# Performance work log

Hardware: AMD Instinct MI355X
Metric: run time of the kernel (lower is better)

Reference implementation:

```python
import jax, jax.numpy as jnp
import numpy as np

N = 50000
E = 800000
D_IN = 64
D_H = 64


def setup_inputs() -> dict:
    key = jax.random.key(0)
    k1, k2, k3, k4 = jax.random.split(key, 4)
    x = jax.random.normal(k1, (N, D_IN), dtype=jnp.float32)
    edge_index = jax.random.randint(k2, (2, E), 0, N, dtype=jnp.int32)
    W1 = jax.random.normal(k3, (D_IN, D_H), dtype=jnp.float32) * (1.0 / np.sqrt(D_IN))
    b1 = jnp.zeros((D_H,), dtype=jnp.float32)
    W2 = jax.random.normal(k4, (D_H, 1), dtype=jnp.float32) * (1.0 / np.sqrt(D_H))
    b2 = jnpp = jnp.zeros((1,), dtype=jnp.float32)
    return {"x": x, "edge_index": edge_index, "W1": W1, "b1": b1, "W2": W2, "b2": b2}


def reference(x, edge_index, W1, b1, W2, b2):
    n = x.shape[0]
    # dgl.add_self_loop: append (i, i) edges for every node
    loops = jnp.arange(n, dtype=edge_index.dtype)
    src = jnp.concatenate([edge_index[0], loops])
    dst = jnp.concatenate([edge_index[1], loops])

    ones = jnp.ones(src.shape[0], dtype=x.dtype)
    deg_out = jax.ops.segment_sum(ones, src, num_segments=n)  # out-degree (src side)
    deg_in = jax.ops.segment_sum(ones, dst, num_segments=n)   # in-degree (dst side)
    # norm='both': symmetric D^{-1/2} A D^{-1/2}; zero where degree is zero (DGL sets inf->0)
    norm_src = jnp.where(deg_out > 0, jax.lax.rsqrt(deg_out), 0.0)[:, None]
    norm_dst = jnp.where(deg_in > 0, jax.lax.rsqrt(deg_in), 0.0)[:, None]

    def aggregate(h):
        # degree-normalized sparse neighbor sum (SpMM via gather + segment_sum)
        h = h * norm_src
        m = jax.ops.segment_sum(h[src], dst, num_segments=n)
        return m * norm_dst

    # layer 1 (in_feats == h_feats -> aggregate first, then transform), bias after agg
    h = aggregate(x) @ W1 + b1
    h = jax.nn.relu(h)
    # layer 2 (in_feats > out_feats -> transform first, then aggregate), bias at end
    out = aggregate(h @ W2) + b2
    return out  # [N, 1]
```

## Files before the change

kernel.cpp:

```cpp
#include <hip/hip_runtime.h>


constexpr int D = 64;
constexpr int NODE_TILE = 12800;
constexpr int NCHUNK = 64;
constexpr int HTH = 1024;

typedef float f32x8 __attribute__((ext_vector_type(8)));

__device__ __forceinline__ int rl_i(int v, int l) { return __builtin_amdgcn_readlane(v, l); }
__device__ __forceinline__ float rl_f(float v, int l) {
    return __builtin_bit_cast(float, __builtin_amdgcn_readlane(__builtin_bit_cast(int, v), l));
}

__global__ void __launch_bounds__(HTH) k_hist_lds(
        const int* __restrict__ src, const int* __restrict__ dst,
        unsigned int* __restrict__ part, int e, int ce) {
    __shared__ unsigned int h[NODE_TILE];
    int b = blockIdx.x;
    int v0 = blockIdx.y * NODE_TILE;
    for (int i = threadIdx.x; i < NODE_TILE; i += HTH) h[i] = 0u;
    __syncthreads();
    int lo = b * ce, hi = min(lo + ce, e);
    for (int i = lo + threadIdx.x; i < hi; i += HTH) {
        unsigned int us = (unsigned int)(src[i] - v0);
        if (us < (unsigned int)NODE_TILE) atomicAdd(&h[us], 1u);
        unsigned int ud = (unsigned int)(dst[i] - v0);
        if (ud < (unsigned int)NODE_TILE) atomicAdd(&h[ud], 0x10000u);
    }
    __syncthreads();
    unsigned int* p = part + ((size_t)blockIdx.y * NCHUNK + b) * NODE_TILE;
    for (int i = threadIdx.x; i < NODE_TILE; i += HTH) p[i] = h[i];
}

__global__ void k_merge_scan(const unsigned int* __restrict__ part,
                             unsigned short* __restrict__ colpref,
                             int* __restrict__ cnt_out, int* __restrict__ cnt_in,
                             int* __restrict__ cursor, int* __restrict__ bsum, int n) {
    __shared__ int s[256];
    int tid = threadIdx.x;
    int v = blockIdx.x * 256 + tid;
    int ci = 0;
    if (v < n) {
        int pass = v / NODE_TILE;
        int vl = v - pass * NODE_TILE;
        const unsigned int* p = part + (size_t)pass * NCHUNK * NODE_TILE + vl;
        unsigned int tot = 0, run_in = 0;
        for (int b = 0; b < NCHUNK; ++b) {
            colpref[(size_t)b * n + v] = (unsigned short)run_in;
            unsigned int t = p[(size_t)b * NODE_TILE];
            tot += t;
            run_in += t >> 16;
        }
        cnt_out[v] = (int)(tot & 0xFFFFu);
        ci = (int)(tot >> 16);
        cnt_in[v] = ci;
    }
    s[tid] = ci;
    __syncthreads();
#pragma unroll
    for (int off = 1; off < 256; off <<= 1) {
        int t = (tid >= off) ? s[tid - off] : 0;
        __syncthreads();
        s[tid] += t;
        __syncthreads();
    }
    if (v < n) cursor[v] = s[tid] - ci;
    if (tid == 255) bsum[blockIdx.x] = s[255];
}

__global__ void k_scan_bsum(int* __restrict__ bsum, int nb) {
    __shared__ int s[256];
    __shared__ int carry;
    int tid = threadIdx.x;
    if (tid == 0) carry = 0;
    __syncthreads();
    for (int start = 0; start < nb; start += 256) {
        int i = start + tid;
        int v = (i < nb) ? bsum[i] : 0;
        s[tid] = v;
        __syncthreads();
#pragma unroll
        for (int off = 1; off < 256; off <<= 1) {
            int t = (tid >= off) ? s[tid - off] : 0;
            __syncthreads();
            s[tid] += t;
            __syncthreads();
        }
        if (i < nb) bsum[i] = s[tid] - v + carry;
        __syncthreads();
        if (tid == 0) carry += s[255];
        __syncthreads();
    }
}

__global__ void k_finalize(const int* __restrict__ cnt_out, const int* __restrict__ cnt_in,
                           const int* __restrict__ bsum,
                           int* __restrict__ cursor, int4* __restrict__ meta, int n) {
    int i = blockIdx.x * blockDim.x + threadIdx.x;
    if (i >= n) return;
    int start = cursor[i] + bsum[i >> 8];
    cursor[i] = start;
    meta[i] = make_int4(start, cnt_in[i], cnt_out[i], 0);
}

__global__ void __launch_bounds__(HTH) k_bin_lds(
        const int* __restrict__ src, const int* __restrict__ dst,
        const int* __restrict__ start, const unsigned short* __restrict__ colpref,
        const int* __restrict__ cnt_out,
        unsigned int* __restrict__ col, int e, int n, int ce) {
    __shared__ int cur[NODE_TILE];
    int b = blockIdx.x;
    int v0 = blockIdx.y * NODE_TILE;
    int vcnt = min(NODE_TILE, n - v0);
    for (int i = threadIdx.x; i < vcnt; i += HTH)
        cur[i] = start[v0 + i] + (int)colpref[(size_t)b * n + v0 + i];
    __syncthreads();
    int lo = b * ce, hi = min(lo + ce, e);
    for (int i = lo + threadIdx.x; i < hi; i += HTH) {
        int d = dst[i];
        unsigned int ud = (unsigned int)(d - v0);
        if (ud < (unsigned int)NODE_TILE) {
            int s = src[i];
            int p = atomicAdd(&cur[ud], 1);
            col[p] = (unsigned int)s | ((unsigned int)cnt_out[s] << 16);
        }
    }
}

__global__ void __launch_bounds__(256) k_gemm(
        const float* __restrict__ x, const float* __restrict__ W1,
        float* __restrict__ y, int n) {
    __shared__ float sW1[D * D];
    int tid = threadIdx.x;
    for (int i = tid; i < D * D; i += 256) sW1[i] = W1[i];
    __syncthreads();

    int lane = tid & 63;
    int wv = __builtin_amdgcn_readfirstlane(tid >> 6);
    int r0 = (blockIdx.x * 4 + wv) * 8;
    if (r0 >= n) return;

    float acc[8];
#pragma unroll
    for (int i = 0; i < 8; ++i) acc[i] = 0.0f;

    if (r0 + 8 <= n) {
        const float* xw = x + (size_t)r0 * D;
#pragma unroll
        for (int kt = 0; kt < 8; ++kt) {
            const float* p = xw + kt * 8;
            f32x8 X0, X1, X2, X3, X4, X5, X6, X7;
            asm volatile(
                "s_load_dwordx8 %0, %8, 0x0\n\t"
                "s_load_dwordx8 %1, %8, 0x100\n\t"
                "s_load_dwordx8 %2, %8, 0x200\n\t"
                "s_load_dwordx8 %3, %8, 0x300\n\t"
                "s_load_dwordx8 %4, %8, 0x400\n\t"
                "s_load_dwordx8 %5, %8, 0x500\n\t"
                "s_load_dwordx8 %6, %8, 0x600\n\t"
                "s_load_dwordx8 %7, %8, 0x700\n\t"
                "s_waitcnt lgkmcnt(0)"
                : "=s"(X0), "=s"(X1), "=s"(X2), "=s"(X3),
                  "=s"(X4), "=s"(X5), "=s"(X6), "=s"(X7)
                : "s"(p));
#pragma unroll
            for (int j = 0; j < 8; ++j) {
                float wk = sW1[(kt * 8 + j) * D + lane];
                acc[0] = fmaf(X0[j], wk, acc[0]);
                acc[1] = fmaf(X1[j], wk, acc[1]);
                acc[2] = fmaf(X2[j], wk, acc[2]);
                acc[3] = fmaf(X3[j], wk, acc[3]);
                acc[4] = fmaf(X4[j], wk, acc[4]);
                acc[5] = fmaf(X5[j], wk, acc[5]);
                acc[6] = fmaf(X6[j], wk, acc[6]);
                acc[7] = fmaf(X7[j], wk, acc[7]);
            }
        }
#pragma unroll
        for (int i = 0; i < 8; ++i)
            y[(size_t)(r0 + i) * D + lane] = acc[i];
    } else {
        float xr[8];
#pragma unroll
        for (int i = 0; i < 8; ++i) {
            int r = r0 + i;
            xr[i] = (r < n) ? x[(size_t)r * D + lane] : 0.0f;
        }
#pragma unroll
        for (int k = 0; k < D; ++k) {
            float wk = sW1[k * D + lane];
#pragma unroll
            for (int i = 0; i < 8; ++i)
                acc[i] = fmaf(rl_f(xr[i], k), wk, acc[i]);
        }
#pragma unroll
        for (int i = 0; i < 8; ++i) {
            int r = r0 + i;
            if (r < n) y[(size_t)r * D + lane] = acc[i];
        }
    }
}

__global__ void __launch_bounds__(256) k_node(
        const float* __restrict__ y, const int4* __restrict__ meta,
        const unsigned int* __restrict__ col,
        const float* __restrict__ b1, const float* __restrict__ W2,
        float* __restrict__ zs, int n) {
    int tid = threadIdx.x;
    int wave = tid >> 6;
    int lane = tid & 63;
    float b1v = b1[lane];
    float w2v = W2[lane];

    int nwaves = gridDim.x * 4;
    int node = blockIdx.x * 4 + wave;
    if (node >= n) return;
    int4 mt = meta[node];

    while (true) {
        int nxt = node + nwaves;
        int4 mt_nx = make_int4(0, 0, 0, 0);
        if (nxt < n) mt_nx = meta[nxt];

        int base = mt.x;
        int cnt = mt.y;
        float nd = rsqrtf((float)(mt.y + 1));
        float ns = rsqrtf((float)(mt.z + 1));

        float a0 = ns * y[(size_t)node * D + lane];
        float a1 = 0.0f, a2 = 0.0f, a3 = 0.0f;

        for (int b0 = 0; b0 < cnt; b0 += 64) {
            int m = cnt - b0; if (m > 64) m = 64;
            unsigned int cw = (lane < m) ? col[base + b0 + lane] : 0u;
            int idx = (int)(cw & 0xFFFFu);
            float w = rsqrtf((float)(cw >> 16) + 1.0f);
            int j = 0;
            for (; j + 8 <= m; j += 8) {
                int s0 = rl_i(idx, j + 0), s1 = rl_i(idx, j + 1);
                int s2 = rl_i(idx, j + 2), s3 = rl_i(idx, j + 3);
                int s4 = rl_i(idx, j + 4), s5 = rl_i(idx, j + 5);
                int s6 = rl_i(idx, j + 6), s7 = rl_i(idx, j + 7);
                float x0 = y[(size_t)s0 * D + lane];
                float x1 = y[(size_t)s1 * D + lane];
                float x2 = y[(size_t)s2 * D + lane];
                float x3 = y[(size_t)s3 * D + lane];
                float x4 = y[(size_t)s4 * D + lane];
                float x5 = y[(size_t)s5 * D + lane];
                float x6 = y[(size_t)s6 * D + lane];
                float x7 = y[(size_t)s7 * D + lane];
                a0 = fmaf(rl_f(w, j + 0), x0, a0);
                a1 = fmaf(rl_f(w, j + 1), x1, a1);
                a2 = fmaf(rl_f(w, j + 2), x2, a2);
                a3 = fmaf(rl_f(w, j + 3), x3, a3);
                a0 = fmaf(rl_f(w, j + 4), x4, a0);
                a1 = fmaf(rl_f(w, j + 5), x5, a1);
                a2 = fmaf(rl_f(w, j + 6), x6, a2);
                a3 = fmaf(rl_f(w, j + 7), x7, a3);
            }
            for (; j < m; ++j)
                a0 = fmaf(rl_f(w, j), y[(size_t)rl_i(idx, j) * D + lane], a0);
        }

        float h = fmaxf(((a0 + a1) + (a2 + a3)) * nd + b1v, 0.0f);
        float zp = h * w2v;
#pragma unroll
        for (int off = 32; off > 0; off >>= 1) zp += __shfl_down(zp, off);
        if (lane == 0) zs[node] = zp * ns;

        if (nxt >= n) break;
        node = nxt;
        mt = mt_nx;
    }
}

__global__ void k_out(const float* __restrict__ zs,
                      const int4* __restrict__ meta, const unsigned int* __restrict__ col,
                      const float* __restrict__ b2,
                      float* __restrict__ out, int n) {
    int g = blockIdx.x * blockDim.x + threadIdx.x;
    int node = g >> 3;
    int sub = g & 7;
    if (node >= n) return;
    int4 mt = meta[node];
    int base = mt.x;
    int c = mt.y;
    float s = (sub == 0) ? zs[node] : 0.0f;
    for (int j = sub; j < c; j += 8) s += zs[col[base + j] & 0xFFFFu];
    s += __shfl_xor(s, 1);
    s += __shfl_xor(s, 2);
    s += __shfl_xor(s, 4);
    if (sub == 0) {
        float nd = rsqrtf((float)(mt.y + 1));
        out[node] = nd * s + b2[0];
    }
}

extern "C" void kernel_launch(void* const* d_in, const int* in_sizes, int n_in,
                              void* d_out, int out_size, void* d_ws, size_t ws_size,
                              hipStream_t stream) {
    const float* x  = (const float*)d_in[0];
    const int*   ei = (const int*)d_in[1];
    const float* W1 = (const float*)d_in[2];
    const float* b1 = (const float*)d_in[3];
    const float* W2 = (const float*)d_in[4];
    const float* b2 = (const float*)d_in[5];
    float* out = (float*)d_out;

    const int n = in_sizes[0] / D;
    const int e = in_sizes[1] / 2;
    const int* src = ei;
    const int* dst = ei + e;

    const int nb = (n + 255) / 256;
    const int npass = (n + NODE_TILE - 1) / NODE_TILE;
    const int ce = (e + NCHUNK - 1) / NCHUNK;

    char* ws = (char*)d_ws;
    int*   cnt_out = (int*)ws;   ws += sizeof(int) * (size_t)n;
    int*   cnt_in  = (int*)ws;   ws += sizeof(int) * (size_t)n;
    int*   cursor  = (int*)ws;   ws += sizeof(int) * (size_t)n;
    int*   bsum    = (int*)ws;   ws += sizeof(int) * (size_t)((nb + 255) & ~255);
    int4*  meta    = (int4*)ws;  ws += sizeof(int4) * (size_t)n;
    unsigned short* colpref = (unsigned short*)ws;
    ws += sizeof(unsigned short) * (size_t)NCHUNK * n;
    unsigned int* col = (unsigned int*)ws;  ws += sizeof(unsigned int) * (size_t)e;
    size_t part_bytes = sizeof(unsigned int) * (size_t)npass * NCHUNK * NODE_TILE;
    size_t y_bytes    = sizeof(float) * (size_t)n * D;
    unsigned int* part = (unsigned int*)ws;
    float* y = (float*)ws;
    ws += (part_bytes > y_bytes ? part_bytes : y_bytes);
    float* zs = (float*)cnt_in;

    const int B = 256;

    k_hist_lds<<<dim3(NCHUNK, npass), HTH, 0, stream>>>(src, dst, part, e, ce);
    k_merge_scan<<<nb, 256, 0, stream>>>(part, colpref, cnt_out, cnt_in, cursor, bsum, n);
    k_scan_bsum<<<1, 256, 0, stream>>>(bsum, nb);
    k_finalize<<<(n + B - 1) / B, B, 0, stream>>>(cnt_out, cnt_in, bsum, cursor, meta, n);
    k_bin_lds<<<dim3(NCHUNK, npass), HTH, 0, stream>>>(src, dst, cursor, colpref,
                                                       cnt_out, col, e, n, ce);
    k_gemm<<<(n + 31) / 32, B, 0, stream>>>(x, W1, y, n);
    k_node<<<2048, B, 0, stream>>>(y, meta, col, b1, W2, zs, n);
    k_out<<<((size_t)n * 8 + B - 1) / B, B, 0, stream>>>(zs, meta, col, b2, out, n);
}
```

Before: 111.0 us.

## Fuse histogram with GEMM launch and fold finalize into binning kernel

Merges the edge-degree histogram and the dense x@W1 transform into a single launch, with blocks split by index, so the independent GEMM work overlaps the atomic-heavy histogram. Folds the finalize step into the binning kernel: each block computes global start offsets inline and chunk 0 writes the meta records. This removes two kernel launches and their serialization gaps. In exchange, y and zs get their own workspace regions instead of aliasing, and GEMM blocks now use 1024 threads with the 51 KB dynamic LDS sized for the histogram, which may reduce GEMM occupancy.

```diff
diff --git a/kernel.cpp b/kernel.cpp
--- a/kernel.cpp
+++ b/kernel.cpp
@@ -13,24 +13,102 @@
     return __builtin_bit_cast(float, __builtin_amdgcn_readlane(__builtin_bit_cast(int, v), l));
 }
 
-__global__ void __launch_bounds__(HTH) k_hist_lds(
+__global__ void __launch_bounds__(HTH) k_hist_gemm(
         const int* __restrict__ src, const int* __restrict__ dst,
-        unsigned int* __restrict__ part, int e, int ce) {
-    __shared__ unsigned int h[NODE_TILE];
-    int b = blockIdx.x;
-    int v0 = blockIdx.y * NODE_TILE;
-    for (int i = threadIdx.x; i < NODE_TILE; i += HTH) h[i] = 0u;
-    __syncthreads();
-    int lo = b * ce, hi = min(lo + ce, e);
-    for (int i = lo + threadIdx.x; i < hi; i += HTH) {
-        unsigned int us = (unsigned int)(src[i] - v0);
-        if (us < (unsigned int)NODE_TILE) atomicAdd(&h[us], 1u);
-        unsigned int ud = (unsigned int)(dst[i] - v0);
-        if (ud < (unsigned int)NODE_TILE) atomicAdd(&h[ud], 0x10000u);
-    }
-    __syncthreads();
-    unsigned int* p = part + ((size_t)blockIdx.y * NCHUNK + b) * NODE_TILE;
-    for (int i = threadIdx.x; i < NODE_TILE; i += HTH) p[i] = h[i];
+        unsigned int* __restrict__ part, int e, int ce, int hblocks,
+        const float* __restrict__ x, const float* __restrict__ W1,
+        float* __restrict__ y, int n) {
+    extern __shared__ char smem[];
+    int tid = threadIdx.x;
+
+    if (blockIdx.x < (unsigned)hblocks) {
+        unsigned int* h = (unsigned int*)smem;
+        int b = blockIdx.x & (NCHUNK - 1);
+        int pass = blockIdx.x >> 6;
+        int v0 = pass * NODE_TILE;
+        for (int i = tid; i < NODE_TILE; i += HTH) h[i] = 0u;
+        __syncthreads();
+        int lo = b * ce, hi = min(lo + ce, e);
+        for (int i = lo + tid; i < hi; i += HTH) {
+            unsigned int us = (unsigned int)(src[i] - v0);
+            if (us < (unsigned int)NODE_TILE) atomicAdd(&h[us], 1u);
+            unsigned int ud = (unsigned int)(dst[i] - v0);
+            if (ud < (unsigned int)NODE_TILE) atomicAdd(&h[ud], 0x10000u);
+        }
+        __syncthreads();
+        unsigned int* p = part + ((size_t)pass * NCHUNK + b) * NODE_TILE;
+        for (int i = tid; i < NODE_TILE; i += HTH) p[i] = h[i];
+    } else {
+        float* sW1 = (float*)smem;
+        for (int i = tid; i < D * D; i += HTH) sW1[i] = W1[i];
+        __syncthreads();
+
+        int lane = tid & 63;
+        int wv = __builtin_amdgcn_readfirstlane(tid >> 6);
+        int gb = blockIdx.x - hblocks;
+        int r0 = (gb * 16 + wv) * 8;
+        if (r0 >= n) return;
+
+        float acc[8];
+#pragma unroll
+        for (int i = 0; i < 8; ++i) acc[i] = 0.0f;
+
+        if (r0 + 8 <= n) {
+            const float* xw = x + (size_t)r0 * D;
+#pragma unroll
+            for (int kt = 0; kt < 8; ++kt) {
+                const float* p = xw + kt * 8;
+                f32x8 X0, X1, X2, X3, X4, X5, X6, X7;
+                asm volatile(
+                    "s_load_dwordx8 %0, %8, 0x0\n\t"
+                    "s_load_dwordx8 %1, %8, 0x100\n\t"
+                    "s_load_dwordx8 %2, %8, 0x200\n\t"
+                    "s_load_dwordx8 %3, %8, 0x300\n\t"
+                    "s_load_dwordx8 %4, %8, 0x400\n\t"
+                    "s_load_dwordx8 %5, %8, 0x500\n\t"
+                    "s_load_dwordx8 %6, %8, 0x600\n\t"
+                    "s_load_dwordx8 %7, %8, 0x700\n\t"
+                    "s_waitcnt lgkmcnt(0)"
+                    : "=s"(X0), "=s"(X1), "=s"(X2), "=s"(X3),
+                      "=s"(X4), "=s"(X5), "=s"(X6), "=s"(X7)
+                    : "s"(p));
+#pragma unroll
+                for (int j = 0; j < 8; ++j) {
+                    float wk = sW1[(kt * 8 + j) * D + lane];
+                    acc[0] = fmaf(X0[j], wk, acc[0]);
+                    acc[1] = fmaf(X1[j], wk, acc[1]);
+                    acc[2] = fmaf(X2[j], wk, acc[2]);
+                    acc[3] = fmaf(X3[j], wk, acc[3]);
+                    acc[4] = fmaf(X4[j], wk, acc[4]);
+                    acc[5] = fmaf(X5[j], wk, acc[5]);
+                    acc[6] = fmaf(X6[j], wk, acc[6]);
+                    acc[7] = fmaf(X7[j], wk, acc[7]);
+                }
+            }
+#pragma unroll
+            for (int i = 0; i < 8; ++i)
+                y[(size_t)(r0 + i) * D + lane] = acc[i];
+        } else {
+            float xr[8];
+#pragma unroll
+            for (int i = 0; i < 8; ++i) {
+                int r = r0 + i;
+                xr[i] = (r < n) ? x[(size_t)r * D + lane] : 0.0f;
+            }
+#pragma unroll
+            for (int k = 0; k < D; ++k) {
+                float wk = sW1[k * D + lane];
+#pragma unroll
+                for (int i = 0; i < 8; ++i)
+                    acc[i] = fmaf(rl_f(xr[i], k), wk, acc[i]);
+            }
+#pragma unroll
+            for (int i = 0; i < 8; ++i) {
+                int r = r0 + i;
+                if (r < n) y[(size_t)r * D + lane] = acc[i];
+            }
+        }
+    }
 }
 
 __global__ void k_merge_scan(const unsigned int* __restrict__ part,
@@ -94,27 +172,23 @@
     }
 }
 
-__global__ void k_finalize(const int* __restrict__ cnt_out, const int* __restrict__ cnt_in,
-                           const int* __restrict__ bsum,
-                           int* __restrict__ cursor, int4* __restrict__ meta, int n) {
-    int i = blockIdx.x * blockDim.x + threadIdx.x;
-    if (i >= n) return;
-    int start = cursor[i] + bsum[i >> 8];
-    cursor[i] = start;
-    meta[i] = make_int4(start, cnt_in[i], cnt_out[i], 0);
-}
-
 __global__ void __launch_bounds__(HTH) k_bin_lds(
         const int* __restrict__ src, const int* __restrict__ dst,
-        const int* __restrict__ start, const unsigned short* __restrict__ colpref,
-        const int* __restrict__ cnt_out,
-        unsigned int* __restrict__ col, int e, int n, int ce) {
+        const int* __restrict__ cursor, const int* __restrict__ bsum,
+        const unsigned short* __restrict__ colpref,
+        const int* __restrict__ cnt_out, const int* __restrict__ cnt_in,
+        unsigned int* __restrict__ col, int4* __restrict__ meta,
+        int e, int n, int ce) {
     __shared__ int cur[NODE_TILE];
     int b = blockIdx.x;
     int v0 = blockIdx.y * NODE_TILE;
     int vcnt = min(NODE_TILE, n - v0);
-    for (int i = threadIdx.x; i < vcnt; i += HTH)
-        cur[i] = start[v0 + i] + (int)colpref[(size_t)b * n + v0 + i];
+    for (int i = threadIdx.x; i < vcnt; i += HTH) {
+        int v = v0 + i;
+        int gs = cursor[v] + bsum[v >> 8];
+        cur[i] = gs + (int)colpref[(size_t)b * n + v];
+        if (b == 0) meta[v] = make_int4(gs, cnt_in[v], cnt_out[v], 0);
+    }
     __syncthreads();
     int lo = b * ce, hi = min(lo + ce, e);
     for (int i = lo + threadIdx.x; i < hi; i += HTH) {
@@ -124,80 +198,6 @@
             int s = src[i];
             int p = atomicAdd(&cur[ud], 1);
             col[p] = (unsigned int)s | ((unsigned int)cnt_out[s] << 16);
-        }
-    }
-}
-
-__global__ void __launch_bounds__(256) k_gemm(
-        const float* __restrict__ x, const float* __restrict__ W1,
-        float* __restrict__ y, int n) {
-    __shared__ float sW1[D * D];
-    int tid = threadIdx.x;
-    for (int i = tid; i < D * D; i += 256) sW1[i] = W1[i];
-    __syncthreads();
-
-    int lane = tid & 63;
-    int wv = __builtin_amdgcn_readfirstlane(tid >> 6);
-    int r0 = (blockIdx.x * 4 + wv) * 8;
-    if (r0 >= n) return;
-
-    float acc[8];
-#pragma unroll
-    for (int i = 0; i < 8; ++i) acc[i] = 0.0f;
-
-    if (r0 + 8 <= n) {
-        const float* xw = x + (size_t)r0 * D;
-#pragma unroll
-        for (int kt = 0; kt < 8; ++kt) {
-            const float* p = xw + kt * 8;
-            f32x8 X0, X1, X2, X3, X4, X5, X6, X7;
-            asm volatile(
-                "s_load_dwordx8 %0, %8, 0x0\n\t"
-                "s_load_dwordx8 %1, %8, 0x100\n\t"
-                "s_load_dwordx8 %2, %8, 0x200\n\t"
-                "s_load_dwordx8 %3, %8, 0x300\n\t"
-                "s_load_dwordx8 %4, %8, 0x400\n\t"
-                "s_load_dwordx8 %5, %8, 0x500\n\t"
-                "s_load_dwordx8 %6, %8, 0x600\n\t"
-                "s_load_dwordx8 %7, %8, 0x700\n\t"
-                "s_waitcnt lgkmcnt(0)"
-                : "=s"(X0), "=s"(X1), "=s"(X2), "=s"(X3),
-                  "=s"(X4), "=s"(X5), "=s"(X6), "=s"(X7)
-                : "s"(p));
-#pragma unroll
-            for (int j = 0; j < 8; ++j) {
-                float wk = sW1[(kt * 8 + j) * D + lane];
-                acc[0] = fmaf(X0[j], wk, acc[0]);
-                acc[1] = fmaf(X1[j], wk, acc[1]);
-                acc[2] = fmaf(X2[j], wk, acc[2]);
-                acc[3] = fmaf(X3[j], wk, acc[3]);
-                acc[4] = fmaf(X4[j], wk, acc[4]);
-                acc[5] = fmaf(X5[j], wk, acc[5]);
-                acc[6] = fmaf(X6[j], wk, acc[6]);
-                acc[7] = fmaf(X7[j], wk, acc[7]);
-            }
-        }
-#pragma unroll
-        for (int i = 0; i < 8; ++i)
-            y[(size_t)(r0 + i) * D + lane] = acc[i];
-    } else {
-        float xr[8];
-#pragma unroll
-        for (int i = 0; i < 8; ++i) {
-            int r = r0 + i;
-            xr[i] = (r < n) ? x[(size_t)r * D + lane] : 0.0f;
-        }
-#pragma unroll
-        for (int k = 0; k < D; ++k) {
-            float wk = sW1[k * D + lane];
-#pragma unroll
-            for (int i = 0; i < 8; ++i)
-                acc[i] = fmaf(rl_f(xr[i], k), wk, acc[i]);
-        }
-#pragma unroll
-        for (int i = 0; i < 8; ++i) {
-            int r = r0 + i;
-            if (r < n) y[(size_t)r * D + lane] = acc[i];
         }
     }
 }
@@ -316,6 +316,8 @@
     const int nb = (n + 255) / 256;
     const int npass = (n + NODE_TILE - 1) / NODE_TILE;
     const int ce = (e + NCHUNK - 1) / NCHUNK;
+    const int hblocks = NCHUNK * npass;
+    const int gblocks = (n + 127) / 128;
 
     char* ws = (char*)d_ws;
     int*   cnt_out = (int*)ws;   ws += sizeof(int) * (size_t)n;
@@ -326,22 +328,20 @@
     unsigned short* colpref = (unsigned short*)ws;
     ws += sizeof(unsigned short) * (size_t)NCHUNK * n;
     unsigned int* col = (unsigned int*)ws;  ws += sizeof(unsigned int) * (size_t)e;
-    size_t part_bytes = sizeof(unsigned int) * (size_t)npass * NCHUNK * NODE_TILE;
-    size_t y_bytes    = sizeof(float) * (size_t)n * D;
     unsigned int* part = (unsigned int*)ws;
-    float* y = (float*)ws;
-    ws += (part_bytes > y_bytes ? part_bytes : y_bytes);
-    float* zs = (float*)cnt_in;
+    ws += sizeof(unsigned int) * (size_t)npass * NCHUNK * NODE_TILE;
+    float* y  = (float*)ws;      ws += sizeof(float) * (size_t)n * D;
+    float* zs = (float*)ws;      ws += sizeof(float) * (size_t)n;
 
     const int B = 256;
-
-    k_hist_lds<<<dim3(NCHUNK, npass), HTH, 0, stream>>>(src, dst, part, e, ce);
+    const size_t smem = (size_t)NODE_TILE * sizeof(unsigned int);
+
+    k_hist_gemm<<<hblocks + gblocks, HTH, smem, stream>>>(
+        src, dst, part, e, ce, hblocks, x, W1, y, n);
     k_merge_scan<<<nb, 256, 0, stream>>>(part, colpref, cnt_out, cnt_in, cursor, bsum, n);
     k_scan_bsum<<<1, 256, 0, stream>>>(bsum, nb);
-    k_finalize<<<(n + B - 1) / B, B, 0, stream>>>(cnt_out, cnt_in, bsum, cursor, meta, n);
-    k_bin_lds<<<dim3(NCHUNK, npass), HTH, 0, stream>>>(src, dst, cursor, colpref,
-                                                       cnt_out, col, e, n, ce);
-    k_gemm<<<(n + 31) / 32, B, 0, stream>>>(x, W1, y, n);
+    k_bin_lds<<<dim3(NCHUNK, npass), HTH, 0, stream>>>(
+        src, dst, cursor, bsum, colpref, cnt_out, cnt_in, col, meta, e, n, ce);
     k_node<<<2048, B, 0, stream>>>(y, meta, col, b1, W2, zs, n);
     k_out<<<((size_t)n * 8 + B - 1) / B, B, 0, stream>>>(zs, meta, col, b2, out, n);
 }
```

After: 105.6 us. 4.9% less time.
